# Kernel optimization log

Measured on AMD Instinct MI355X. Metric: run time of the kernel, lower is better.

The kernel has to match this reference:

```python
import jax, jax.numpy as jnp
import numpy as np

BN_EPS = 1e-5


def setup_inputs() -> dict:
    key = jax.random.key(0)
    ks = jax.random.split(key, 11)
    C, P = 256, 128  # inplanes, planes = inplanes // 2
    B, H, W = 4, 64, 64
    s = 0.01  # conv weight init std in the original module
    return {
        "x": jax.random.normal(ks[0], (B, C, H, W), jnp.float32),
        "Wt": jax.random.normal(ks[1], (P, C), jnp.float32) * s,
        "bt": jnp.zeros((P,), jnp.float32),
        "Wp": jax.random.normal(ks[2], (P, C), jnp.float32) * s,
        "bp": jnp.zeros((P,), jnp.float32),
        "Wg": jax.random.normal(ks[3], (P, C), jnp.float32) * s,
        "bg": jnp.zeros((P,), jnp.float32),
        "Wz": jax.random.normal(ks[4], (C, P), jnp.float32) * s,
        "bz": jnp.zeros((C,), jnp.float32),
        "gamma": jax.random.uniform(ks[5], (C,), jnp.float32),
        "beta": jax.random.normal(ks[6], (C,), jnp.float32) * 0.01,
    }


def reference(x, Wt, bt, Wp, bp, Wg, bg, Wz, bz, gamma, beta):
    b, c, h, w = x.shape
    n = h * w
    xf = x.reshape(b, c, n)  # (b, c, n)
    # 1x1 conv projections == per-pixel matmuls
    t = jnp.einsum("pc,bcn->bnp", Wt, xf) + bt            # (b, n, p) queries
    p = jnp.einsum("pc,bcn->bpn", Wp, xf) + bp[:, None]   # (b, p, n) keys
    g = jnp.einsum("pc,bcn->bnp", Wg, xf) + bg            # (b, n, p) values
    planes = Wt.shape[0]
    scale = jnp.asarray(planes, x.dtype) ** 0.5
    att = jnp.einsum("bnp,bpm->bnm", t, p) / scale        # (b, n, n)
    att = jax.nn.softmax(att, axis=-1)                    # softmax over dim 2
    y = jnp.einsum("bnm,bmp->bnp", att, g)                # (b, n, p)
    z = jnp.einsum("cp,bnp->bcn", Wz, y) + bz[:, None]    # (b, c, n)
    z = z.reshape(b, c, h, w)
    # BatchNorm2d, training-mode batch statistics over (B, H, W)
    mean = z.mean(axis=(0, 2, 3))
    var = z.var(axis=(0, 2, 3))
    zn = (z - mean[:, None, None]) * jax.lax.rsqrt(var + BN_EPS)[:, None, None]
    out = zn * gamma[:, None, None] + beta[:, None, None] + x
    return out
```

## Files before the change

kernel.cpp:

```cpp
#include <hip/hip_runtime.h>


#define SCALE_ 0.08838834764831845f

typedef __bf16 bf16x8 __attribute__((ext_vector_type(8)));
typedef float f32x4 __attribute__((ext_vector_type(4)));
typedef unsigned short ushort8v __attribute__((ext_vector_type(8)));

__device__ inline unsigned short f2bf(float f) {
  unsigned int u = __float_as_uint(f);
  u += 0x7fffu + ((u >> 16) & 1u);
  return (unsigned short)(u >> 16);
}
__device__ inline float bflo(unsigned int u) { return __uint_as_float(u << 16); }
__device__ inline float bfhi(unsigned int u) { return __uint_as_float(u & 0xffff0000u); }

__device__ inline void gl16(const unsigned short* g, unsigned short* l) {
  __builtin_amdgcn_global_load_lds(
      (const __attribute__((address_space(1))) unsigned int*)(g),
      (__attribute__((address_space(3))) unsigned int*)(l), 16, 0, 0);
}

__global__ __launch_bounds__(256) void prep_kernel(
    const float* __restrict__ x,
    const float* __restrict__ Wt, const float* __restrict__ Wp, const float* __restrict__ Wg,
    unsigned short* __restrict__ xT, unsigned short* __restrict__ Wb) {
  const int tid = threadIdx.x;
  const int bx = blockIdx.x, b = blockIdx.y;
  if (bx >= 64) {
    if (b != 0) return;
#pragma unroll
    for (int it = 0; it < 3; ++it) {
      int k = (bx - 64) * 256 + tid + it * 4096;
      const float* src = (k < 4096 ? Wt : (k < 8192 ? Wp : Wg)) + (size_t)(k & 4095) * 8;
      float4 a = *(const float4*)src, c = *(const float4*)(src + 4);
      ushort8v us;
      us[0] = f2bf(a.x); us[1] = f2bf(a.y); us[2] = f2bf(a.z); us[3] = f2bf(a.w);
      us[4] = f2bf(c.x); us[5] = f2bf(c.y); us[6] = f2bf(c.z); us[7] = f2bf(c.w);
      *(ushort8v*)(Wb + (size_t)k * 8) = us;
    }
    return;
  }
  __shared__ float sT[128 * 68];
  const int w = tid >> 6, l = tid & 63;
  const int n0 = bx * 64;
  for (int half = 0; half < 2; ++half) {
    if (half) __syncthreads();
#pragma unroll
    for (int it = 0; it < 8; ++it) {
      int e = it * 256 + tid;
      int c = e >> 4, n4 = e & 15;
      float4 v = *(const float4*)(x + (size_t)(b * 256 + half * 128 + c) * 4096 + n0 + n4 * 4);
      *(float4*)(sT + c * 68 + n4 * 4) = v;
    }
    __syncthreads();
#pragma unroll
    for (int it = 0; it < 4; ++it) {
      int c8 = it * 4 + w;
      int n = l;
      ushort8v us;
#pragma unroll
      for (int j = 0; j < 8; ++j) us[j] = f2bf(sT[(c8 * 8 + j) * 68 + n]);
      *(ushort8v*)(xT + (size_t)b * 1048576 + (size_t)(n0 + n) * 256 + half * 128 + c8 * 8) = us;
    }
  }
}

__global__ __launch_bounds__(256, 3) void proj_kernel(
    const unsigned short* __restrict__ xT, const unsigned short* __restrict__ Wb,
    const float* __restrict__ bt, const float* __restrict__ bp, const float* __restrict__ bg,
    unsigned short* __restrict__ Qb, unsigned short* __restrict__ Kb,
    unsigned short* __restrict__ Vtb) {
  __shared__ unsigned short sX[64 * 256];
  __shared__ unsigned short sW[128 * 64];
  const int tid = threadIdx.x;
  const int w = tid >> 6, l = tid & 63;
  const int l15 = l & 15, lh = l >> 4;
  const int n0 = blockIdx.x * 64;
  const int b = blockIdx.y;
  const int sel = blockIdx.z;
  const unsigned short* xTb = xT + (size_t)b * 1048576;
  const unsigned short* Ws = Wb + (size_t)sel * 32768;
#pragma unroll
  for (int it = 0; it < 8; ++it) {
    int row = w * 16 + it * 2 + (l >> 5);
    int s = l & 31;
    int src = (s & 24) | ((s & 7) ^ (row & 7));
    gl16(xTb + (size_t)(n0 + row) * 256 + src * 8, sX + (w * 16 + it * 2) * 256);
  }
  f32x4 acc[2][4];
#pragma unroll
  for (int mt = 0; mt < 2; ++mt)
#pragma unroll
    for (int nt = 0; nt < 4; ++nt) acc[mt][nt] = (f32x4){0.f, 0.f, 0.f, 0.f};

  for (int ko4 = 0; ko4 < 4; ++ko4) {
    __syncthreads();
#pragma unroll
    for (int it = 0; it < 4; ++it) {
      int p = w * 32 + it * 8 + (l >> 3);
      int s = l & 7;
      gl16(Ws + (size_t)p * 256 + ko4 * 64 + ((s ^ (p & 7)) * 8),
           sW + (w * 32 + it * 8) * 64);
    }
    __syncthreads();
#pragma unroll
    for (int ko2 = 0; ko2 < 2; ++ko2) {
      bf16x8 af[2];
#pragma unroll
      for (int mt = 0; mt < 2; ++mt) {
        int p = w * 32 + mt * 16 + l15;
        af[mt] = *(const bf16x8*)(sW + p * 64 + (((ko2 * 4 + lh) ^ (p & 7)) << 3));
      }
#pragma unroll
      for (int nt = 0; nt < 4; ++nt) {
        int n = nt * 16 + l15;
        int ci = ko4 * 8 + ko2 * 4 + lh;
        int slot = (ci & 24) | ((ci & 7) ^ (n & 7));
        bf16x8 bfv = *(const bf16x8*)(sX + n * 256 + (slot << 3));
#pragma unroll
        for (int mt = 0; mt < 2; ++mt)
          acc[mt][nt] = __builtin_amdgcn_mfma_f32_16x16x32_bf16(af[mt], bfv, acc[mt][nt], 0, 0, 0);
      }
    }
  }
  const float* bias = sel == 0 ? bt : (sel == 1 ? bp : bg);
  const float scl = sel == 0 ? SCALE_ : 1.0f;
#pragma unroll
  for (int mt = 0; mt < 2; ++mt) {
    int pb = w * 32 + mt * 16 + lh * 4;
    float4 bv = *(const float4*)(bias + pb);
    const float* bvf = (const float*)&bv;
    if (sel < 2) {
      unsigned short* dst = (sel == 0 ? Qb : Kb) + (size_t)b * 524288;
#pragma unroll
      for (int nt = 0; nt < 4; ++nt) {
        ushort4 us;
        us.x = f2bf((acc[mt][nt][0] + bv.x) * scl);
        us.y = f2bf((acc[mt][nt][1] + bv.y) * scl);
        us.z = f2bf((acc[mt][nt][2] + bv.z) * scl);
        us.w = f2bf((acc[mt][nt][3] + bv.w) * scl);
        *(ushort4*)(dst + (size_t)(n0 + nt * 16 + l15) * 128 + pb) = us;
      }
    } else {
      unsigned short* dst = Vtb + (size_t)b * 524288;
#pragma unroll
      for (int nt = 0; nt < 4; ++nt)
#pragma unroll
        for (int r = 0; r < 4; ++r)
          dst[(size_t)(pb + r) * 4096 + n0 + nt * 16 + l15] = f2bf(acc[mt][nt][r] + bvf[r]);
    }
  }
}

__global__ __launch_bounds__(256, 2) void attn_kernel(
    const unsigned short* __restrict__ Qb, const unsigned short* __restrict__ Kb,
    const unsigned short* __restrict__ Vtb, unsigned short* __restrict__ Ytp,
    float* __restrict__ denp) {
  __shared__ unsigned short sm[40960];
  const int tid = threadIdx.x;
  const int w = tid >> 6, l = tid & 63;
  const int l15 = l & 15, lh = l >> 4;
  const int b = blockIdx.y, sp = blockIdx.z;
  const int n0 = blockIdx.x * 128;
  const int kvbase = sp * 1024;

  bf16x8 qf0[4], qf1[4];
  {
    const unsigned short* q0 = Qb + (size_t)(b * 4096 + n0 + w * 32 + l15) * 128 + lh * 8;
    const unsigned short* q1 = q0 + 16 * 128;
#pragma unroll
    for (int ko = 0; ko < 4; ++ko) {
      qf0[ko] = *(const bf16x8*)(q0 + ko * 32);
      qf1[ko] = *(const bf16x8*)(q1 + ko * 32);
    }
  }
  unsigned short* sPw = sm + 32768 + w * 2048;

  f32x4 yacc0[8], yacc1[8];
#pragma unroll
  for (int i = 0; i < 8; ++i) {
    yacc0[i] = (f32x4){0.f, 0.f, 0.f, 0.f};
    yacc1[i] = (f32x4){0.f, 0.f, 0.f, 0.f};
  }
  float den0 = 0.f, den1 = 0.f;

  const unsigned short* Kbase = Kb + (size_t)(b * 4096 + kvbase) * 128;
  const unsigned short* Vbase = Vtb + (size_t)(b * 128) * 4096 + kvbase;

#define STAGE(T, BUFO)                                                              \
  {                                                                                 \
    const int koff_ = (T) * 64;                                                     \
    _Pragma("unroll")                                                               \
    for (int it = 0; it < 4; ++it) {                                                \
      int krow = w * 16 + it * 4 + (l >> 4);                                        \
      gl16(Kbase + (size_t)(koff_ + krow) * 128 + (((l & 15) ^ (krow & 7)) << 3),   \
           sm + (BUFO) + (w * 16 + it * 4) * 128);                                  \
      int vrow = w * 32 + it * 8 + (l >> 3);                                        \
      gl16(Vbase + (size_t)vrow * 4096 + koff_ + (((l & 7) ^ (vrow & 7)) << 3),     \
           sm + 16384 + (BUFO) + (w * 32 + it * 8) * 64);                           \
    }                                                                               \
  }

  STAGE(0, 0)
  for (int t = 0; t < 16; ++t) {
    const int co = (t & 1) * 8192;
    unsigned short* kb = sm + co;
    unsigned short* vb = sm + 16384 + co;
    __syncthreads();
    if (t + 1 < 16) {
      STAGE(t + 1, co ^ 8192)
    }
    f32x4 sacc0[4], sacc1[4];
#pragma unroll
    for (int mt = 0; mt < 4; ++mt) {
      sacc0[mt] = (f32x4){0.f, 0.f, 0.f, 0.f};
      sacc1[mt] = (f32x4){0.f, 0.f, 0.f, 0.f};
    }
    __builtin_amdgcn_s_setprio(1);
#pragma unroll
    for (int ko = 0; ko < 4; ++ko) {
#pragma unroll
      for (int mt = 0; mt < 4; ++mt) {
        int m = mt * 16 + l15;
        bf16x8 ak = *(const bf16x8*)(kb + m * 128 + (((lh + 4 * ko) ^ (m & 7)) << 3));
        sacc0[mt] = __builtin_amdgcn_mfma_f32_16x16x32_bf16(ak, qf0[ko], sacc0[mt], 0, 0, 0);
        sacc1[mt] = __builtin_amdgcn_mfma_f32_16x16x32_bf16(ak, qf1[ko], sacc1[mt], 0, 0, 0);
      }
    }
    __builtin_amdgcn_s_setprio(0);
#define SOFTMAX_SET(SACC, ROWB, DEN)                                                \
    {                                                                               \
      float rs = 0.f;                                                               \
      _Pragma("unroll")                                                             \
      for (int mt = 0; mt < 4; ++mt) {                                              \
        float e0 = __expf(SACC[mt][0]);                                             \
        float e1 = __expf(SACC[mt][1]);                                             \
        float e2 = __expf(SACC[mt][2]);                                             \
        float e3 = __expf(SACC[mt][3]);                                             \
        rs += (e0 + e1) + (e2 + e3);                                                \
        ushort4 us;                                                                 \
        us.x = f2bf(e0); us.y = f2bf(e1); us.z = f2bf(e2); us.w = f2bf(e3);         \
        int mblk = mt * 2 + (lh >> 1);                                              \
        *(ushort4*)(sPw + ((ROWB) + l15) * 64 + ((mblk ^ (l15 & 7)) << 3) +         \
                    (lh & 1) * 4) = us;                                             \
      }                                                                             \
      rs += __shfl_xor(rs, 16);                                                     \
      rs += __shfl_xor(rs, 32);                                                     \
      DEN += rs;                                                                    \
    }
    SOFTMAX_SET(sacc0, 0, den0)
    SOFTMAX_SET(sacc1, 16, den1)
    __builtin_amdgcn_s_setprio(1);
#pragma unroll
    for (int ko = 0; ko < 2; ++ko) {
      bf16x8 bp0 = *(const bf16x8*)(sPw + l15 * 64 + (((lh + 4 * ko) ^ (l15 & 7)) << 3));
      bf16x8 bp1 = *(const bf16x8*)(sPw + (16 + l15) * 64 + (((lh + 4 * ko) ^ (l15 & 7)) << 3));
#pragma unroll
      for (int dt = 0; dt < 8; ++dt) {
        int d = dt * 16 + l15;
        bf16x8 av = *(const bf16x8*)(vb + d * 64 + (((lh + 4 * ko) ^ (d & 7)) << 3));
        yacc0[dt] = __builtin_amdgcn_mfma_f32_16x16x32_bf16(av, bp0, yacc0[dt], 0, 0, 0);
        yacc1[dt] = __builtin_amdgcn_mfma_f32_16x16x32_bf16(av, bp1, yacc1[dt], 0, 0, 0);
      }
    }
    __builtin_amdgcn_s_setprio(0);
  }
  {
    unsigned short* Yt = Ytp + (size_t)(sp * 4 + b) * 524288 +
                         (size_t)(n0 + w * 32 + l15) * 128;
#pragma unroll
    for (int dt = 0; dt < 8; ++dt) {
      ushort4 us;
      us.x = f2bf(yacc0[dt][0]); us.y = f2bf(yacc0[dt][1]);
      us.z = f2bf(yacc0[dt][2]); us.w = f2bf(yacc0[dt][3]);
      *(ushort4*)(Yt + dt * 16 + lh * 4) = us;
    }
    unsigned short* Yt1 = Yt + 16 * 128;
#pragma unroll
    for (int dt = 0; dt < 8; ++dt) {
      ushort4 us;
      us.x = f2bf(yacc1[dt][0]); us.y = f2bf(yacc1[dt][1]);
      us.z = f2bf(yacc1[dt][2]); us.w = f2bf(yacc1[dt][3]);
      *(ushort4*)(Yt1 + dt * 16 + lh * 4) = us;
    }
    if (lh == 0) {
      denp[(size_t)(sp * 4 + b) * 4096 + n0 + w * 32 + l15] = den0;
      denp[(size_t)(sp * 4 + b) * 4096 + n0 + w * 32 + 16 + l15] = den1;
    }
  }
}

__global__ __launch_bounds__(256, 4) void zbn_kernel(
    const unsigned short* __restrict__ Ytp, const float* __restrict__ denp,
    const float* __restrict__ Wz, const float* __restrict__ bz,
    float* __restrict__ Z, float* __restrict__ S1p, float* __restrict__ S2p) {
  __shared__ unsigned short sY[64 * 128];
  __shared__ unsigned short sW[64 * 128];
  __shared__ float sDen[64];
  const int tid = threadIdx.x;
  const int w = tid >> 6, l = tid & 63;
  const int l15 = l & 15, lh = l >> 4;
  const int bx = blockIdx.x;
  const int b = blockIdx.y;
  const int n0 = bx * 64;
  const int c0 = blockIdx.z * 64;
  if (tid < 64) {
    float s = 0.f;
#pragma unroll
    for (int sp = 0; sp < 4; ++sp) s += denp[sp * 16384 + b * 4096 + n0 + tid];
    sDen[tid] = 1.0f / s;
  }
  __syncthreads();
#pragma unroll
  for (int it = 0; it < 4; ++it) {
    int e = it * 256 + tid;
    int n = e >> 4, pc = e & 15;
    size_t o = (size_t)b * 524288 + (size_t)(n0 + n) * 128 + pc * 8;
    float a0 = 0, a1 = 0, a2 = 0, a3 = 0, a4 = 0, a5 = 0, a6 = 0, a7 = 0;
#pragma unroll
    for (int sp = 0; sp < 4; ++sp) {
      uint4 v = *(const uint4*)(Ytp + (size_t)sp * 2097152 + o);
      a0 += bflo(v.x); a1 += bfhi(v.x);
      a2 += bflo(v.y); a3 += bfhi(v.y);
      a4 += bflo(v.z); a5 += bfhi(v.z);
      a6 += bflo(v.w); a7 += bfhi(v.w);
    }
    float idn = sDen[n];
    ushort8v us;
    us[0] = f2bf(a0 * idn); us[1] = f2bf(a1 * idn);
    us[2] = f2bf(a2 * idn); us[3] = f2bf(a3 * idn);
    us[4] = f2bf(a4 * idn); us[5] = f2bf(a5 * idn);
    us[6] = f2bf(a6 * idn); us[7] = f2bf(a7 * idn);
    *(ushort8v*)(sY + n * 128 + ((pc ^ (n & 7)) << 3)) = us;
  }
#pragma unroll
  for (int it = 0; it < 4; ++it) {
    int e = it * 256 + tid;
    int c = e >> 4, pc = e & 15;
    const float* wsrc = Wz + (size_t)(c0 + c) * 128 + pc * 8;
    float4 wa = *(const float4*)(wsrc);
    float4 wb = *(const float4*)(wsrc + 4);
    ushort8v us;
    us[0] = f2bf(wa.x); us[1] = f2bf(wa.y); us[2] = f2bf(wa.z); us[3] = f2bf(wa.w);
    us[4] = f2bf(wb.x); us[5] = f2bf(wb.y); us[6] = f2bf(wb.z); us[7] = f2bf(wb.w);
    *(ushort8v*)(sW + c * 128 + ((pc ^ (c & 7)) << 3)) = us;
  }
  __syncthreads();
  f32x4 acc[4];
#pragma unroll
  for (int nt = 0; nt < 4; ++nt) acc[nt] = (f32x4){0.f, 0.f, 0.f, 0.f};
  const int crow = w * 16 + l15;
#pragma unroll
  for (int ko = 0; ko < 4; ++ko) {
    bf16x8 aw = *(const bf16x8*)(sW + crow * 128 + (((lh + 4 * ko) ^ (crow & 7)) << 3));
#pragma unroll
    for (int nt = 0; nt < 4; ++nt) {
      int nrow = nt * 16 + l15;
      bf16x8 by = *(const bf16x8*)(sY + nrow * 128 + (((lh + 4 * ko) ^ (nrow & 7)) << 3));
      acc[nt] = __builtin_amdgcn_mfma_f32_16x16x32_bf16(aw, by, acc[nt], 0, 0, 0);
    }
  }
  const int cb = c0 + w * 16 + lh * 4;
  float4 bzv = *(const float4*)(bz + cb);
  const float* bzf = (const float*)&bzv;
#pragma unroll
  for (int r = 0; r < 4; ++r) {
    float s1 = 0.f, s2 = 0.f;
#pragma unroll
    for (int nt = 0; nt < 4; ++nt) {
      float z = acc[nt][r] + bzf[r];
      Z[(size_t)(b * 256 + cb + r) * 4096 + n0 + nt * 16 + l15] = z;
      s1 += z;
      s2 += z * z;
    }
#pragma unroll
    for (int m = 1; m < 16; m <<= 1) {
      s1 += __shfl_xor(s1, m);
      s2 += __shfl_xor(s2, m);
    }
    if (l15 == 0) {
      S1p[(size_t)(cb + r) * 256 + b * 64 + bx] = s1;
      S2p[(size_t)(cb + r) * 256 + b * 64 + bx] = s2;
    }
  }
}

__global__ __launch_bounds__(256) void bnfin_kernel(
    const float* __restrict__ S1p, const float* __restrict__ S2p,
    const float* __restrict__ gamma, const float* __restrict__ beta,
    float* __restrict__ Scale, float* __restrict__ Shift) {
  __shared__ float r1[4], r2[4];
  const int c = blockIdx.x, tid = threadIdx.x;
  float s1 = S1p[(size_t)c * 256 + tid];
  float s2 = S2p[(size_t)c * 256 + tid];
#pragma unroll
  for (int m = 1; m < 64; m <<= 1) {
    s1 += __shfl_xor(s1, m);
    s2 += __shfl_xor(s2, m);
  }
  if ((tid & 63) == 0) { r1[tid >> 6] = s1; r2[tid >> 6] = s2; }
  __syncthreads();
  if (tid == 0) {
    float S1t = (r1[0] + r1[1]) + (r1[2] + r1[3]);
    float S2t = (r2[0] + r2[1]) + (r2[2] + r2[3]);
    const float inv_cnt = 1.0f / 16384.0f;
    float mean = S1t * inv_cnt;
    float var = fmaxf(S2t * inv_cnt - mean * mean, 0.0f);
    float inv = rsqrtf(var + 1e-5f);
    float sc = gamma[c] * inv;
    Scale[c] = sc;
    Shift[c] = beta[c] - mean * sc;
  }
}

__global__ __launch_bounds__(256) void out_kernel(
    const float* __restrict__ Z, const float* __restrict__ x,
    const float* __restrict__ Scale, const float* __restrict__ Shift,
    float* __restrict__ out) {
  int i4 = blockIdx.x * 256 + threadIdx.x;
  int flat = i4 << 2;
  int c = (flat >> 12) & 255;
  float4 z = *(const float4*)(Z + flat);
  float4 xv = *(const float4*)(x + flat);
  float sc = Scale[c], sh = Shift[c];
  float4 o;
  o.x = z.x * sc + sh + xv.x;
  o.y = z.y * sc + sh + xv.y;
  o.z = z.z * sc + sh + xv.z;
  o.w = z.w * sc + sh + xv.w;
  *(float4*)(out + flat) = o;
}

extern "C" void kernel_launch(void* const* d_in, const int* in_sizes, int n_in,
                              void* d_out, int out_size, void* d_ws, size_t ws_size,
                              hipStream_t stream) {
  (void)in_sizes; (void)n_in; (void)out_size; (void)ws_size;
  const float* x = (const float*)d_in[0];
  const float* Wt = (const float*)d_in[1];
  const float* bt = (const float*)d_in[2];
  const float* Wp = (const float*)d_in[3];
  const float* bp = (const float*)d_in[4];
  const float* Wg = (const float*)d_in[5];
  const float* bg = (const float*)d_in[6];
  const float* Wz = (const float*)d_in[7];
  const float* bz = (const float*)d_in[8];
  const float* gamma = (const float*)d_in[9];
  const float* beta = (const float*)d_in[10];

  unsigned short* Qb = (unsigned short*)d_ws;
  unsigned short* Kb = Qb + 2097152;
  unsigned short* Vtb = Kb + 2097152;
  unsigned short* Ytp = Vtb + 2097152;
  float* denp = (float*)(Ytp + 8388608);
  float* Z = denp + 65536;
  float* Scale = Z + 4194304;
  float* Shift = Scale + 256;

  unsigned short* xT = (unsigned short*)Z;
  unsigned short* Wb = (unsigned short*)denp;
  float* S1p = (float*)Qb;
  float* S2p = S1p + 65536;

  prep_kernel<<<dim3(80, 4), 256, 0, stream>>>(x, Wt, Wp, Wg, xT, Wb);
  proj_kernel<<<dim3(64, 4, 3), 256, 0, stream>>>(xT, Wb, bt, bp, bg, Qb, Kb, Vtb);
  attn_kernel<<<dim3(32, 4, 4), 256, 0, stream>>>(Qb, Kb, Vtb, Ytp, denp);
  zbn_kernel<<<dim3(64, 4, 4), 256, 0, stream>>>(Ytp, denp, Wz, bz, Z, S1p, S2p);
  bnfin_kernel<<<256, 256, 0, stream>>>(S1p, S2p, gamma, beta, Scale, Shift);
  out_kernel<<<4096, 256, 0, stream>>>(Z, x, Scale, Shift, (float*)d_out);
}
```

Measured before the change: 86.60 us.

## Raise attention KV split to eight and drop LDS double buffering for occupancy

```diff
diff --git a/kernel.cpp b/kernel.cpp
--- a/kernel.cpp
+++ b/kernel.cpp
@@ -153,17 +153,17 @@
   }
 }
 
-__global__ __launch_bounds__(256, 2) void attn_kernel(
+__global__ __launch_bounds__(256, 3) void attn_kernel(
     const unsigned short* __restrict__ Qb, const unsigned short* __restrict__ Kb,
     const unsigned short* __restrict__ Vtb, unsigned short* __restrict__ Ytp,
-    float* __restrict__ denp) {
-  __shared__ unsigned short sm[40960];
+    float* __restrict__ denp, int ntiles) {
+  __shared__ unsigned short sm[24576];
   const int tid = threadIdx.x;
   const int w = tid >> 6, l = tid & 63;
   const int l15 = l & 15, lh = l >> 4;
   const int b = blockIdx.y, sp = blockIdx.z;
   const int n0 = blockIdx.x * 128;
-  const int kvbase = sp * 1024;
+  const int kvbase = sp * (ntiles * 64);
 
   bf16x8 qf0[4], qf1[4];
   {
@@ -175,7 +175,7 @@
       qf1[ko] = *(const bf16x8*)(q1 + ko * 32);
     }
   }
-  unsigned short* sPw = sm + 32768 + w * 2048;
+  unsigned short* sPw = sm + 16384 + w * 2048;
 
   f32x4 yacc0[8], yacc1[8];
 #pragma unroll
@@ -188,29 +188,20 @@
   const unsigned short* Kbase = Kb + (size_t)(b * 4096 + kvbase) * 128;
   const unsigned short* Vbase = Vtb + (size_t)(b * 128) * 4096 + kvbase;
 
-#define STAGE(T, BUFO)                                                              \
-  {                                                                                 \
-    const int koff_ = (T) * 64;                                                     \
-    _Pragma("unroll")                                                               \
-    for (int it = 0; it < 4; ++it) {                                                \
-      int krow = w * 16 + it * 4 + (l >> 4);                                        \
-      gl16(Kbase + (size_t)(koff_ + krow) * 128 + (((l & 15) ^ (krow & 7)) << 3),   \
-           sm + (BUFO) + (w * 16 + it * 4) * 128);                                  \
-      int vrow = w * 32 + it * 8 + (l >> 3);                                        \
-      gl16(Vbase + (size_t)vrow * 4096 + koff_ + (((l & 7) ^ (vrow & 7)) << 3),     \
-           sm + 16384 + (BUFO) + (w * 32 + it * 8) * 64);                           \
-    }                                                                               \
-  }
-
-  STAGE(0, 0)
-  for (int t = 0; t < 16; ++t) {
-    const int co = (t & 1) * 8192;
-    unsigned short* kb = sm + co;
-    unsigned short* vb = sm + 16384 + co;
+  for (int t = 0; t < ntiles; ++t) {
+    const int koff = t * 64;
     __syncthreads();
-    if (t + 1 < 16) {
-      STAGE(t + 1, co ^ 8192)
-    }
+#pragma unroll
+    for (int it = 0; it < 4; ++it) {
+      int krow = w * 16 + it * 4 + (l >> 4);
+      gl16(Kbase + (size_t)(koff + krow) * 128 + (((l & 15) ^ (krow & 7)) << 3),
+           sm + (w * 16 + it * 4) * 128);
+      int vrow = w * 32 + it * 8 + (l >> 3);
+      gl16(Vbase + (size_t)vrow * 4096 + koff + (((l & 7) ^ (vrow & 7)) << 3),
+           sm + 8192 + (w * 32 + it * 8) * 64);
+    }
+    __syncthreads();
+
     f32x4 sacc0[4], sacc1[4];
 #pragma unroll
     for (int mt = 0; mt < 4; ++mt) {
@@ -223,7 +214,7 @@
 #pragma unroll
       for (int mt = 0; mt < 4; ++mt) {
         int m = mt * 16 + l15;
-        bf16x8 ak = *(const bf16x8*)(kb + m * 128 + (((lh + 4 * ko) ^ (m & 7)) << 3));
+        bf16x8 ak = *(const bf16x8*)(sm + m * 128 + (((lh + 4 * ko) ^ (m & 7)) << 3));
         sacc0[mt] = __builtin_amdgcn_mfma_f32_16x16x32_bf16(ak, qf0[ko], sacc0[mt], 0, 0, 0);
         sacc1[mt] = __builtin_amdgcn_mfma_f32_16x16x32_bf16(ak, qf1[ko], sacc1[mt], 0, 0, 0);
       }
@@ -259,7 +250,7 @@
 #pragma unroll
       for (int dt = 0; dt < 8; ++dt) {
         int d = dt * 16 + l15;
-        bf16x8 av = *(const bf16x8*)(vb + d * 64 + (((lh + 4 * ko) ^ (d & 7)) << 3));
+        bf16x8 av = *(const bf16x8*)(sm + 8192 + d * 64 + (((lh + 4 * ko) ^ (d & 7)) << 3));
         yacc0[dt] = __builtin_amdgcn_mfma_f32_16x16x32_bf16(av, bp0, yacc0[dt], 0, 0, 0);
         yacc1[dt] = __builtin_amdgcn_mfma_f32_16x16x32_bf16(av, bp1, yacc1[dt], 0, 0, 0);
       }
@@ -294,7 +285,8 @@
 __global__ __launch_bounds__(256, 4) void zbn_kernel(
     const unsigned short* __restrict__ Ytp, const float* __restrict__ denp,
     const float* __restrict__ Wz, const float* __restrict__ bz,
-    float* __restrict__ Z, float* __restrict__ S1p, float* __restrict__ S2p) {
+    float* __restrict__ Z, float* __restrict__ S1p, float* __restrict__ S2p,
+    int nsplit) {
   __shared__ unsigned short sY[64 * 128];
   __shared__ unsigned short sW[64 * 128];
   __shared__ float sDen[64];
@@ -307,8 +299,7 @@
   const int c0 = blockIdx.z * 64;
   if (tid < 64) {
     float s = 0.f;
-#pragma unroll
-    for (int sp = 0; sp < 4; ++sp) s += denp[sp * 16384 + b * 4096 + n0 + tid];
+    for (int sp = 0; sp < nsplit; ++sp) s += denp[sp * 16384 + b * 4096 + n0 + tid];
     sDen[tid] = 1.0f / s;
   }
   __syncthreads();
@@ -318,8 +309,7 @@
     int n = e >> 4, pc = e & 15;
     size_t o = (size_t)b * 524288 + (size_t)(n0 + n) * 128 + pc * 8;
     float a0 = 0, a1 = 0, a2 = 0, a3 = 0, a4 = 0, a5 = 0, a6 = 0, a7 = 0;
-#pragma unroll
-    for (int sp = 0; sp < 4; ++sp) {
+    for (int sp = 0; sp < nsplit; ++sp) {
       uint4 v = *(const uint4*)(Ytp + (size_t)sp * 2097152 + o);
       a0 += bflo(v.x); a1 += bfhi(v.x);
       a2 += bflo(v.y); a3 += bfhi(v.y);
@@ -435,7 +425,7 @@
 extern "C" void kernel_launch(void* const* d_in, const int* in_sizes, int n_in,
                               void* d_out, int out_size, void* d_ws, size_t ws_size,
                               hipStream_t stream) {
-  (void)in_sizes; (void)n_in; (void)out_size; (void)ws_size;
+  (void)in_sizes; (void)n_in; (void)out_size;
   const float* x = (const float*)d_in[0];
   const float* Wt = (const float*)d_in[1];
   const float* bt = (const float*)d_in[2];
@@ -448,12 +438,17 @@
   const float* gamma = (const float*)d_in[9];
   const float* beta = (const float*)d_in[10];
 
+  const size_t need8 = (size_t)(12 * 1024 * 1024) + (size_t)8 * 4 * 524288 * 2 +
+                       (size_t)8 * 16384 * 4 + (size_t)4194304 * 4 + 4096;
+  const int nsplit = (ws_size >= need8) ? 8 : 4;
+  const int ntiles = (4096 / nsplit) / 64;
+
   unsigned short* Qb = (unsigned short*)d_ws;
   unsigned short* Kb = Qb + 2097152;
   unsigned short* Vtb = Kb + 2097152;
   unsigned short* Ytp = Vtb + 2097152;
-  float* denp = (float*)(Ytp + 8388608);
-  float* Z = denp + 65536;
+  float* denp = (float*)(Ytp + (size_t)nsplit * 4 * 524288);
+  float* Z = denp + (size_t)nsplit * 16384;
   float* Scale = Z + 4194304;
   float* Shift = Scale + 256;
 
@@ -464,8 +459,8 @@
 
   prep_kernel<<<dim3(80, 4), 256, 0, stream>>>(x, Wt, Wp, Wg, xT, Wb);
   proj_kernel<<<dim3(64, 4, 3), 256, 0, stream>>>(xT, Wb, bt, bp, bg, Qb, Kb, Vtb);
-  attn_kernel<<<dim3(32, 4, 4), 256, 0, stream>>>(Qb, Kb, Vtb, Ytp, denp);
-  zbn_kernel<<<dim3(64, 4, 4), 256, 0, stream>>>(Ytp, denp, Wz, bz, Z, S1p, S2p);
+  attn_kernel<<<dim3(32, 4, nsplit), 256, 0, stream>>>(Qb, Kb, Vtb, Ytp, denp, ntiles);
+  zbn_kernel<<<dim3(64, 4, 4), 256, 0, stream>>>(Ytp, denp, Wz, bz, Z, S1p, S2p, nsplit);
   bnfin_kernel<<<256, 256, 0, stream>>>(S1p, S2p, gamma, beta, Scale, Shift);
   out_kernel<<<4096, 256, 0, stream>>>(Z, x, Scale, Shift, (float*)d_out);
 }
```

After: 140.0 us. 61.7% more time.
